# Performance work log

Hardware: AMD Instinct MI355X
Metric: run time of the kernel (lower is better)

Reference implementation:

```python
import jax, jax.numpy as jnp
import numpy as np

# Loihi neuron constants (from netParams['neuron'])
VTH_MANT = 80.0
THETA = VTH_MANT * 64.0          # Loihi threshold = vThMant * 2**6
I_DECAY = 1024.0                 # current decay (of 4096)
V_DECAY = 128.0                  # voltage decay (of 4096)
REF_DELAY = 1.0                  # refractory steps after a spike
W_SCALE = 64.0                   # Loihi weighted-input scaling (2**6)
TAU_RHO = 1.0
POOL_W = 1.1 * VTH_MANT          # slayer pool synapse weight (one spike fires output)


@jax.custom_vjp
def spike(v):
    return (v >= THETA).astype(v.dtype)

def _spike_fwd(v):
    return spike(v), v

def _spike_bwd(v, g):
    # SLAYER surrogate gradient: exponential pdf around threshold
    return (g * jnp.exp(-jnp.abs(v - THETA) / (TAU_RHO * THETA)) / THETA,)

spike.defvjp(_spike_fwd, _spike_bwd)


def loihi_dynamics(wsum):
    """CUBA Loihi LIF over time-leading weighted input wsum: [T, ...] -> spikes [T, ...]."""
    i_dec = (4096.0 - I_DECAY) / 4096.0
    v_dec = (4096.0 - V_DECAY) / 4096.0

    def step(carry, x):
        u, v, ref = carry
        u = i_dec * u + W_SCALE * x                    # synaptic current
        v = jnp.where(ref > 0, 0.0, v_dec * v + u)     # membrane, clamped in refractory
        s = spike(v)
        v = v * (1.0 - s)                              # reset on spike
        ref = jnp.where(s > 0, REF_DELAY, jnp.maximum(ref - 1.0, 0.0))
        return (u, v, ref), s

    z = jnp.zeros_like(wsum[0])
    _, s = jax.lax.scan(step, (z, z, z), wsum)
    return s


def delay_shift(s):
    # slayer.delayShift(spike, 1): shift spike train by 1 timestep (time-leading axis)
    return jnp.concatenate([jnp.zeros_like(s[:1]), s[:-1]], axis=0)


def conv2d_t(x, w, pad):
    # x: [T, B, C, H, W]; fold T into batch for the spatial conv
    T, B, C, H, W = x.shape
    y = jax.lax.conv_general_dilated(
        x.reshape(T * B, C, H, W), w, (1, 1), [(pad, pad), (pad, pad)],
        dimension_numbers=('NCHW', 'OIHW', 'NCHW'))
    return y.reshape(T, B, y.shape[1], y.shape[2], y.shape[3])


def sum_pool(x, k):
    # slayer pool: per-channel sum pooling with fixed synaptic weight POOL_W
    y = jax.lax.reduce_window(x, 0.0, jax.lax.add,
                              (1, 1, 1, k, k), (1, 1, 1, k, k), 'VALID')
    return POOL_W * y


def setup_inputs() -> dict:
    key = jax.random.key(0)
    ks = jax.random.split(key, 6)
    B, C, H, W, T = 48, 4, 26, 26, 128
    # Bernoulli(0.1) spike trains
    spike_input = (jax.random.uniform(ks[0], (B, C, H, W, T)) < 0.1).astype(jnp.float32)
    w_conv1 = jax.random.normal(ks[1], (8, 4, 5, 5), jnp.float32) * 4.0
    w_conv2 = jax.random.normal(ks[2], (16, 8, 3, 3), jnp.float32) * 4.0
    w_conv3 = jax.random.normal(ks[3], (32, 16, 3, 3), jnp.float32) * 4.0
    w_fc1 = jax.random.normal(ks[4], (512, 3 * 3 * 32), jnp.float32) * 4.0
    w_fc2 = jax.random.normal(ks[5], (2, 512), jnp.float32) * 4.0
    return {"spike_input": spike_input, "w_conv1": w_conv1, "w_conv2": w_conv2,
            "w_conv3": w_conv3, "w_fc1": w_fc1, "w_fc2": w_fc2}


def reference(spike_input, w_conv1, w_conv2, w_conv3, w_fc1, w_fc2):
    x = jnp.transpose(spike_input, (4, 0, 1, 2, 3))  # [T, B, C, H, W]

    def block(x, w, pad):
        s = delay_shift(loihi_dynamics(conv2d_t(x, w, pad)))
        s = delay_shift(loihi_dynamics(sum_pool(s, 2)))
        return s  # dropout is identity in eval

    x = block(x, w_conv1, 1)   # 26 -> 24 -> 12
    x = block(x, w_conv2, 1)   # 12 -> 12 -> 6
    x = block(x, w_conv3, 1)   # 6 -> 6 -> 3
    T, B = x.shape[0], x.shape[1]
    x = x.reshape(T, B, -1)    # [T, B, 32*3*3] (C,H,W flatten order matches torch view)
    s = delay_shift(loihi_dynamics(jnp.einsum('tbi,oi->tbo', x, w_fc1)))
    s = delay_shift(loihi_dynamics(jnp.einsum('tbi,oi->tbo', s, w_fc2)))
    return jnp.transpose(s, (1, 2, 0))  # [B, 2, T]
```

## Files before the change

kernel.cpp:

```cpp
#include <hip/hip_runtime.h>


#define THETA 5120.0f

typedef __attribute__((ext_vector_type(8))) short bfrag;
typedef __attribute__((ext_vector_type(4))) float ffrag;

__device__ __forceinline__ float dyn_step(float x, float& u, float& v, float& r) {
#pragma clang fp contract(off)
    u = 0.75f * u + 64.0f * x;
    float vn = 0.96875f * v + u;
    vn = (r > 0.0f) ? 0.0f : vn;
    float s;
    if (vn >= THETA) { s = 1.0f; v = 0.0f; r = 1.0f; }
    else             { s = 0.0f; v = vn; r = fmaxf(r - 1.0f, 0.0f); }
    return s;
}

__device__ __forceinline__ float dpp_add_xor1(float x) {
    int y = __builtin_amdgcn_update_dpp(0, __float_as_int(x), 0xB1, 0xF, 0xF, true);
    return x + __int_as_float(y);
}
__device__ __forceinline__ float dpp_add_xor2(float x) {
    int y = __builtin_amdgcn_update_dpp(0, __float_as_int(x), 0x4E, 0xF, 0xF, true);
    return x + __int_as_float(y);
}

__device__ __forceinline__ unsigned int compress4(unsigned long long x) {
    x &= 0x1111111111111111ull;
    x = (x | (x >> 3))  & 0x0303030303030303ull;
    x = (x | (x >> 6))  & 0x000F000F000F000Full;
    x = (x | (x >> 12)) & 0x000000FF000000FFull;
    x = (x | (x >> 24)) & 0xFFFFull;
    return (unsigned int)x;
}

__device__ __forceinline__ unsigned short f2bf(float f) {
    unsigned int u = __float_as_uint(f);
    unsigned int r = (u + 0x7FFFu + ((u >> 16) & 1u)) >> 16;
    return (unsigned short)r;
}
__device__ __forceinline__ float bf2f(unsigned short b) {
    return __uint_as_float(((unsigned int)b) << 16);
}

__device__ __forceinline__ float f4_elem(float4 v, int j) {
    return (j == 0) ? v.x : (j == 1) ? v.y : (j == 2) ? v.z : v.w;
}

__global__ __launch_bounds__(256) void k_masks(const float* __restrict__ in,
                                               const float* __restrict__ wfc1,
                                               uint2* __restrict__ xb,
                                               unsigned short* __restrict__ wb) {
    if (blockIdx.x >= 624) {
        int gid = (blockIdx.x - 624) * 256 + threadIdx.x;
        int o = gid / 288, k = gid % 288;
        float w = wfc1[gid];
        unsigned short b0 = f2bf(w);
        float r1 = w - bf2f(b0);
        unsigned short b1 = f2bf(r1);
        float r2 = r1 - bf2f(b1);
        unsigned short b2 = f2bf(r2);
        size_t ob = (size_t)o * 864 + k;
        wb[ob]       = b0;
        wb[ob + 288] = b1;
        wb[ob + 576] = b2;
        return;
    }
    int wv = blockIdx.x * 4 + (threadIdx.x >> 6);
    int lane = threadIdx.x & 63;
    int y = wv % 26; int r = wv / 26;
    int pr = r & 1; int b = r >> 1;
    int ch = lane >> 5;
    int x = lane & 31;
    int act = x < 26;
    int xc = act ? x : 25;
    const float4* src = (const float4*)(in + (size_t)(((b * 4 + pr * 2 + ch) * 26 + y) * 26 + xc) * 128);
    uint2* dst = xb + ((size_t)b * 2 + pr) * 28 + (y + 1);
    if (y == 0) {
        uint2* pp = xb + ((size_t)b * 2 + pr) * 28;
        uint2 z = make_uint2(0u, 0u);
#pragma unroll
        for (int h = 0; h < 2; ++h) {
            int t = h * 64 + lane;
            pp[(size_t)t * 2688] = z;
            pp[(size_t)t * 2688 + 27] = z;
        }
    }
    for (int t4 = 0; t4 < 32; ++t4) {
        float4 f = src[t4];
#pragma unroll
        for (int k = 0; k < 4; ++k) {
            float fv = f4_elem(f, k);
            unsigned long long bal = __ballot(act && (fv != 0.0f));
            if (lane == 0) {
                unsigned int lo = ((unsigned int)bal & 0x03FFFFFFu) << 1;
                unsigned int hi = ((unsigned int)(bal >> 32) & 0x03FFFFFFu) << 1;
                dst[(size_t)(t4 * 4 + k) * 2688] = make_uint2(lo, hi);
            }
        }
    }
}

__global__ __launch_bounds__(576) void k_wsum1(const uint2* __restrict__ xb,
                                               const float* __restrict__ w1,
                                               float* __restrict__ ws) {
    __shared__ float wsh[400];
    __shared__ ffrag tbl4[660];
    int tid = threadIdx.x;
    int H = blockIdx.x & 1;
    int bid = blockIdx.x >> 1;
    int tch = bid & 15;
    int b = bid >> 4;
    float* wsH = ws + (size_t)H * 14155776;
    if (tid < 400) wsh[tid] = w1[H * 400 + tid];
    __syncthreads();
    for (int e = tid; e < 660; e += 576) {
        int ch = e / 165;
        int rem = e % 165;
        int ky = rem / 33;
        int idx = rem % 33;
        ffrag val = {0.f, 0.f, 0.f, 0.f};
#pragma unroll
        for (int oc4 = 0; oc4 < 4; ++oc4) {
            float a = 0.f;
#pragma unroll
            for (int k = 0; k < 5; ++k)
                a += ((idx >> k) & 1) ? wsh[oc4 * 100 + ch * 25 + ky * 5 + k] : 0.f;
            val[oc4] = a;
        }
        tbl4[(ch * 5 + ky) * 33 + idx] = val;
    }
    __syncthreads();
    int q = tid >> 2, s = tid & 3;
    int ox = (q % 12) * 2 + (s & 1);
    int oy = (q / 12) * 2 + (s >> 1);
    int t0 = tch * 8;
    ffrag acc[8];
#pragma unroll
    for (int j = 0; j < 8; ++j) {
        int t = t0 + j;
        const uint2* rp = xb + ((size_t)t * 48 + b) * 56 + oy;
        ffrag a = {0.f, 0.f, 0.f, 0.f};
#pragma unroll
        for (int ky = 0; ky < 5; ++ky) {
            uint2 r0 = rp[ky];
            uint2 r1 = rp[28 + ky];
            a += tbl4[ky * 33 + (int)((r0.x >> ox) & 31u)];
            a += tbl4[(5 + ky) * 33 + (int)((r0.y >> ox) & 31u)];
            a += tbl4[(10 + ky) * 33 + (int)((r1.x >> ox) & 31u)];
            a += tbl4[(15 + ky) * 33 + (int)((r1.y >> ox) & 31u)];
        }
        acc[j] = a;
    }
    size_t tilebase = (size_t)(t0 >> 4) * 1769472 + (t0 & 15);
#pragma unroll
    for (int oc4 = 0; oc4 < 4; ++oc4) {
        float* wp = wsH + tilebase + (size_t)((b * 4 + oc4) * 576 + tid) * 16;
        *(float4*)(wp)     = make_float4(acc[0][oc4], acc[1][oc4], acc[2][oc4], acc[3][oc4]);
        *(float4*)(wp + 4) = make_float4(acc[4][oc4], acc[5][oc4], acc[6][oc4], acc[7][oc4]);
    }
}

__global__ __launch_bounds__(256) void k_scan1(const float* __restrict__ ws,
                                               unsigned short* __restrict__ st1) {
    int wv = blockIdx.x * 4 + (threadIdx.x >> 6);
    int lane = threadIdx.x & 63;
    int H = (wv >= 1728) ? 1 : 0;
    int wvl = wv - H * 1728;
    const float* bp = ws + (size_t)H * 14155776 + (size_t)(wvl * 64 + lane) * 16;
    unsigned short* so = st1 + (size_t)wv * 128;
    float u = 0.f, v = 0.f, rf = 0.f;
    float pu = 0.f, pv = 0.f, prf = 0.f;
    float sp = 0.f;
    unsigned int mb[4];
    float4 cur[4], nxt[4];
#pragma unroll
    for (int i = 0; i < 4; ++i) cur[i] = *(const float4*)(bp + i * 4);
    for (int tb = 0; tb < 8; ++tb) {
        if (tb < 7) {
            const float* np = bp + (size_t)(tb + 1) * 1769472;
#pragma unroll
            for (int i = 0; i < 4; ++i) nxt[i] = *(const float4*)(np + i * 4);
        }
#pragma unroll
        for (int j = 0; j < 16; ++j) {
            int t = tb * 16 + j;
            float w = f4_elem(cur[j >> 2], j & 3);
            float cnt = dpp_add_xor2(dpp_add_xor1(sp));
            float ps = dyn_step(88.0f * cnt, pu, pv, prf);
            unsigned long long bal = __ballot(((lane & 3) == 0) && (ps > 0.5f));
            unsigned int m = compress4(bal);
            int sl = (t >> 1) & 3;
            mb[sl] = (t & 1) ? (mb[sl] | (m << 16)) : m;
            if ((t & 7) == 7 && lane == 0)
                *(uint4*)(so + (t & ~7)) = make_uint4(mb[0], mb[1], mb[2], mb[3]);
            sp = dyn_step(w, u, v, rf);
        }
        if (tb < 7) {
#pragma unroll
            for (int i = 0; i < 4; ++i) cur[i] = nxt[i];
        }
    }
}

__global__ __launch_bounds__(256) void k_mb1(const unsigned short* __restrict__ st1,
                                             unsigned short* __restrict__ pb16) {
    int gid = blockIdx.x * 256 + threadIdx.x;
    int oc = gid & 7; int r = gid >> 3;
    int y = r % 12; r /= 12;
    int b = r % 48; int t = r / 48;
    int base = (oc >> 2) * 1728 + (b * 4 + (oc & 3)) * 9;
    int Q0 = y * 12;
    int w0 = Q0 >> 4, off = Q0 & 15;
    unsigned int v0 = st1[(size_t)(base + w0) * 128 + t];
    unsigned int v1 = (off > 4) ? (unsigned int)st1[(size_t)(base + w0 + 1) * 128 + t] : 0u;
    unsigned int m = ((v0 >> off) | (v1 << (16 - off))) & 0xFFFu;
    size_t rowb = (size_t)(t * 48 + b) * 14;
    pb16[(rowb + y + 1) * 8 + oc] = (unsigned short)(m << 1);
    if (y == 0)  pb16[rowb * 8 + oc] = 0;
    if (y == 11) pb16[(rowb + 13) * 8 + oc] = 0;
}

__global__ __launch_bounds__(576) void k_wsum2(const unsigned short* __restrict__ pb16,
                                               const float* __restrict__ w2,
                                               float* __restrict__ ws) {
    __shared__ float wsh[288];
    __shared__ ffrag tbl4[852];
    int tid = threadIdx.x;
    int tch = blockIdx.x & 3;
    int r = blockIdx.x >> 2;
    int ocg = r & 3; int b = r >> 2;
    if (tid < 288) wsh[tid] = w2[(ocg * 4 + tid / 72) * 72 + (tid % 72)];
    __syncthreads();
    for (int e = tid; e < 852; e += 576) {
        int pr = e / 213;
        int rem = e % 213;
        int ky = rem / 71;
        int idx = rem % 71;
        int lo = idx % 9, hi = idx / 9;
        ffrag val = {0.f, 0.f, 0.f, 0.f};
#pragma unroll
        for (int oc4 = 0; oc4 < 4; ++oc4) {
            float a = 0.f;
#pragma unroll
            for (int k = 0; k < 3; ++k)
                a += ((lo >> k) & 1) ? wsh[oc4 * 72 + (2 * pr) * 9 + ky * 3 + k] : 0.f;
#pragma unroll
            for (int k = 0; k < 3; ++k)
                a += ((hi >> k) & 1) ? wsh[oc4 * 72 + (2 * pr + 1) * 9 + ky * 3 + k] : 0.f;
            val[oc4] = a;
        }
        tbl4[(pr * 3 + ky) * 71 + idx] = val;
    }
    __syncthreads();
    int tq = tid / 144;
    int pix = tid % 144;
    int q = pix >> 2, s = pix & 3;
    int ox = (q % 6) * 2 + (s & 1);
    int oy = (q / 6) * 2 + (s >> 1);
    int t0 = tch * 32 + tq * 8;
    ffrag acc[8];
#pragma unroll
    for (int j = 0; j < 8; ++j) {
        int t = t0 + j;
        ffrag a = {0.f, 0.f, 0.f, 0.f};
        if (t > 0) {
            const uint4* rp = (const uint4*)(pb16 + (((size_t)(t - 1) * 48 + b) * 14 + oy) * 8);
#pragma unroll
            for (int ky = 0; ky < 3; ++ky) {
                uint4 row = rp[ky];
                unsigned int wd[4] = {row.x, row.y, row.z, row.w};
#pragma unroll
                for (int pr = 0; pr < 4; ++pr) {
                    unsigned int lo = (wd[pr] >> ox) & 7u;
                    unsigned int hi = (wd[pr] >> (16 + ox)) & 7u;
                    a += tbl4[(pr * 3 + ky) * 71 + (int)(lo + 9u * hi)];
                }
            }
        }
        acc[j] = a;
    }
    size_t tilebase = (size_t)(t0 >> 4) * 1769472 + (t0 & 15);
#pragma unroll
    for (int oc4 = 0; oc4 < 4; ++oc4) {
        int neuron = (b * 16 + ocg * 4 + oc4) * 144 + pix;
        float* wp = ws + tilebase + (size_t)neuron * 16;
        *(float4*)(wp)     = make_float4(acc[0][oc4], acc[1][oc4], acc[2][oc4], acc[3][oc4]);
        *(float4*)(wp + 4) = make_float4(acc[4][oc4], acc[5][oc4], acc[6][oc4], acc[7][oc4]);
    }
}

__global__ __launch_bounds__(576) void k_scan2(const float* __restrict__ ws,
                                               unsigned short* __restrict__ st2) {
    int tid = threadIdx.x;
    int wloc = tid >> 6, lane = tid & 63;
    int g4 = blockIdx.x;
    const float* bp = ws + (size_t)(g4 * 576 + tid) * 16;
    unsigned short* so = st2 + ((size_t)(g4 * 9 + wloc)) * 128;
    float u = 0.f, v = 0.f, rf = 0.f;
    float pu = 0.f, pv = 0.f, prf = 0.f;
    float sp = 0.f;
    unsigned int mb[4];
    float4 cur[4], nxt[4];
#pragma unroll
    for (int i = 0; i < 4; ++i) cur[i] = *(const float4*)(bp + i * 4);
    for (int tb = 0; tb < 8; ++tb) {
        if (tb < 7) {
            const float* np = bp + (size_t)(tb + 1) * 1769472;
#pragma unroll
            for (int i = 0; i < 4; ++i) nxt[i] = *(const float4*)(np + i * 4);
        }
#pragma unroll
        for (int j = 0; j < 16; ++j) {
            int t = tb * 16 + j;
            float w = f4_elem(cur[j >> 2], j & 3);
            float cnt = dpp_add_xor2(dpp_add_xor1(sp));
            float ps = dyn_step(88.0f * cnt, pu, pv, prf);
            unsigned long long bal = __ballot(((lane & 3) == 0) && (ps > 0.5f));
            unsigned int m = compress4(bal);
            int sl = (t >> 1) & 3;
            mb[sl] = (t & 1) ? (mb[sl] | (m << 16)) : m;
            if ((t & 7) == 7 && lane == 0)
                *(uint4*)(so + (t & ~7)) = make_uint4(mb[0], mb[1], mb[2], mb[3]);
            sp = dyn_step(w, u, v, rf);
        }
        if (tb < 7) {
#pragma unroll
            for (int i = 0; i < 4; ++i) cur[i] = nxt[i];
        }
    }
}

__global__ __launch_bounds__(256) void k_mb2(const unsigned short* __restrict__ st2,
                                             unsigned short* __restrict__ pb2) {
    int gid = blockIdx.x * 256 + threadIdx.x;
    int oc = gid & 15; int r = gid >> 4;
    int y = r % 6; r /= 6;
    int b = r % 48; int t = r / 48;
    int img = b * 16 + oc;
    int g4 = img >> 2, lI = img & 3;
    int Q0 = lI * 36 + y * 6;
    int w0 = Q0 >> 4, off = Q0 & 15;
    unsigned int v0 = st2[(size_t)(g4 * 9 + w0) * 128 + t];
    unsigned int v1 = (off > 10) ? (unsigned int)st2[(size_t)(g4 * 9 + w0 + 1) * 128 + t] : 0u;
    unsigned int m = ((v0 >> off) | (v1 << (16 - off))) & 0x3Fu;
    size_t rowb = (size_t)(t * 48 + b) * 8;
    pb2[(rowb + y + 1) * 16 + oc] = (unsigned short)(m << 1);
    if (y == 0) pb2[rowb * 16 + oc] = 0;
    if (y == 5) pb2[(rowb + 7) * 16 + oc] = 0;
}

__global__ __launch_bounds__(576) void k_wsum3(const unsigned short* __restrict__ pb2,
                                               const float* __restrict__ w3,
                                               float* __restrict__ ws) {
    __shared__ float wsh[576];
    __shared__ ffrag tbl4[1704];
    int tid = threadIdx.x;
    int tch = blockIdx.x & 7;
    int gb = blockIdx.x >> 3;
    int ocg = gb / 12, bg = gb % 12;
    wsh[tid] = w3[(ocg * 4 + tid / 144) * 144 + (tid % 144)];
    __syncthreads();
    for (int e = tid; e < 1536; e += 576) {
        int pr = e / 192;
        int ky = (e / 64) % 3;
        int i = e & 63;
        int lo = i & 7, hi = i >> 3;
        ffrag val = {0.f, 0.f, 0.f, 0.f};
#pragma unroll
        for (int oc4 = 0; oc4 < 4; ++oc4) {
            float a = 0.f;
#pragma unroll
            for (int k = 0; k < 3; ++k)
                a += ((lo >> k) & 1) ? wsh[oc4 * 144 + (2 * pr) * 9 + ky * 3 + k] : 0.f;
#pragma unroll
            for (int k = 0; k < 3; ++k)
                a += ((hi >> k) & 1) ? wsh[oc4 * 144 + (2 * pr + 1) * 9 + ky * 3 + k] : 0.f;
            val[oc4] = a;
        }
        tbl4[(pr * 3 + ky) * 71 + lo + 9 * hi] = val;
    }
    __syncthreads();
    int tq = tid & 3;
    int r = tid >> 2;
    int pix = r % 36;
    int bsel = r / 36;
    int q = pix >> 2, s = pix & 3;
    int ox = (q % 3) * 2 + (s & 1);
    int oy = (q / 3) * 2 + (s >> 1);
    int b = bg * 4 + bsel;
    int t0 = tch * 16 + tq * 4;
    ffrag acc[4];
#pragma unroll
    for (int j = 0; j < 4; ++j) {
        int t = t0 + j;
        ffrag a = {0.f, 0.f, 0.f, 0.f};
        if (t > 0) {
            const uint4* rp = (const uint4*)(pb2 + (((size_t)(t - 1) * 48 + b) * 8 + oy) * 16);
#pragma unroll
            for (int ky = 0; ky < 3; ++ky) {
                uint4 rA = rp[ky * 2];
                uint4 rB = rp[ky * 2 + 1];
                unsigned int wd[8] = {rA.x, rA.y, rA.z, rA.w, rB.x, rB.y, rB.z, rB.w};
#pragma unroll
                for (int pr = 0; pr < 8; ++pr) {
                    unsigned int lo = (wd[pr] >> ox) & 7u;
                    unsigned int hi = (wd[pr] >> (16 + ox)) & 7u;
                    a += tbl4[(pr * 3 + ky) * 71 + (int)(lo + 9u * hi)];
                }
            }
        }
        acc[j] = a;
    }
    size_t base = (size_t)tch * 884736;
#pragma unroll
    for (int oc4 = 0; oc4 < 4; ++oc4) {
        int neuron = (b * 32 + ocg * 4 + oc4) * 36 + pix;
        float* wp = ws + base + (size_t)neuron * 16 + tq * 4;
        *(float4*)(wp) = make_float4(acc[0][oc4], acc[1][oc4], acc[2][oc4], acc[3][oc4]);
    }
}

__global__ __launch_bounds__(256) void k_scan3(const float* __restrict__ ws,
                                               unsigned short* __restrict__ st3) {
    int wv = blockIdx.x * 4 + (threadIdx.x >> 6);
    int lane = threadIdx.x & 63;
    const float* bp = ws + (size_t)(wv * 64 + lane) * 16;
    unsigned short* so = st3 + (size_t)wv * 128;
    float u = 0.f, v = 0.f, rf = 0.f;
    float pu = 0.f, pv = 0.f, prf = 0.f;
    float sp = 0.f;
    unsigned int mb[4];
    float4 cur[4], nxt[4];
#pragma unroll
    for (int i = 0; i < 4; ++i) cur[i] = *(const float4*)(bp + i * 4);
    for (int tb = 0; tb < 8; ++tb) {
        if (tb < 7) {
            const float* np = bp + (size_t)(tb + 1) * 884736;
#pragma unroll
            for (int i = 0; i < 4; ++i) nxt[i] = *(const float4*)(np + i * 4);
        }
#pragma unroll
        for (int j = 0; j < 16; ++j) {
            int t = tb * 16 + j;
            float w = f4_elem(cur[j >> 2], j & 3);
            float cnt = dpp_add_xor2(dpp_add_xor1(sp));
            float ps = dyn_step(88.0f * cnt, pu, pv, prf);
            unsigned long long bal = __ballot(((lane & 3) == 0) && (ps > 0.5f));
            unsigned int m = compress4(bal);
            int sl = (t >> 1) & 3;
            mb[sl] = (t & 1) ? (mb[sl] | (m << 16)) : m;
            if ((t & 7) == 7 && lane == 0)
                *(uint4*)(so + (t & ~7)) = make_uint4(mb[0], mb[1], mb[2], mb[3]);
            sp = dyn_step(w, u, v, rf);
        }
        if (tb < 7) {
#pragma unroll
            for (int i = 0; i < 4; ++i) cur[i] = nxt[i];
        }
    }
}

__global__ __launch_bounds__(256) void k_mb3(const unsigned short* __restrict__ st3,
                                             unsigned short* __restrict__ a3) {
    int gid = blockIdx.x * 256 + threadIdx.x;
    if (gid >= 1755648) return;
    int G = gid % 13824, t = gid / 13824;
    unsigned int bit = ((unsigned int)st3[(size_t)(G >> 4) * 128 + t] >> (G & 15)) & 1u;
    a3[(size_t)(t + 1) * 13824 + G] = bit ? 0x3F80 : 0;
    if (gid < 13824) a3[gid] = 0;
}

__global__ __launch_bounds__(256) void k_fc1mm(const unsigned short* __restrict__ a3,
                                               const unsigned short* __restrict__ wb,
                                               float* __restrict__ wsf1) {
    __shared__ unsigned short Bs[16 * 872];
    int tid = threadIdx.x;
    int nt = blockIdx.x & 31;
    int mc = blockIdx.x >> 5;
    int n0 = nt * 16;
    for (int idx = tid; idx < 13824; idx += 256) {
        int n = idx / 864;
        int kp = idx % 864;
        Bs[n * 872 + kp] = wb[(size_t)(n0 + n) * 864 + kp];
    }
    __syncthreads();
    int wave = tid >> 6;
    int lane = tid & 63;
    int ln = lane & 15, quad = lane >> 4;
#pragma unroll
    for (int i = 0; i < 4; ++i) {
        int m0 = (mc * 16 + wave * 4 + i) * 16;
        const unsigned short* arow = a3 + (size_t)(m0 + ln) * 288 + quad * 8;
        ffrag acc = {0.f, 0.f, 0.f, 0.f};
#pragma unroll
        for (int kb = 0; kb < 9; ++kb) {
            bfrag av = *(const bfrag*)(arow + kb * 32);
#pragma unroll
            for (int c = 0; c < 3; ++c) {
                bfrag bv = *(const bfrag*)(&Bs[ln * 872 + c * 288 + kb * 32 + quad * 8]);
                acc = __builtin_amdgcn_mfma_f32_16x16x32_bf16(av, bv, acc, 0, 0, 0);
            }
        }
        float* wout = wsf1 + (size_t)(m0 + quad * 4) * 512 + n0 + ln;
        wout[0] = acc[0];
        wout[512] = acc[1];
        wout[1024] = acc[2];
        wout[1536] = acc[3];
    }
}

__global__ __launch_bounds__(256) void k_fc1s(const float* __restrict__ wsf1,
                                              float* __restrict__ f1f) {
    int tid = blockIdx.x * 256 + threadIdx.x;
    float u = 0.f, v = 0.f, rf = 0.f;
    float wbuf[16];
#pragma unroll
    for (int i = 0; i < 16; ++i) wbuf[i] = wsf1[(size_t)i * 24576 + tid];
    for (int tb = 0; tb < 128; tb += 16) {
#pragma unroll
        for (int j = 0; j < 16; ++j) {
            int t = tb + j;
            float w = wbuf[j];
            if (t + 16 < 128) wbuf[j] = wsf1[(size_t)(t + 16) * 24576 + tid];
            float s = dyn_step(w, u, v, rf);
            f1f[(size_t)t * 24576 + tid] = s;
        }
    }
}

__global__ __launch_bounds__(256) void k_fc2w(const float* __restrict__ f1f,
                                              const float* __restrict__ wfc2,
                                              float* __restrict__ wsf2) {
    int wv = blockIdx.x * 4 + (threadIdx.x >> 6);
    int lane = threadIdx.x & 63;
    int b = wv % 48, t = wv / 48;
    int o = lane & 1, kq = lane >> 1;
    float acc = 0.f;
    if (t > 0) {
        const float* wp = wfc2 + o * 512 + kq * 16;
        const float* sp = f1f + (size_t)(t - 1) * 24576 + b * 512 + kq * 16;
#pragma unroll
        for (int i = 0; i < 16; ++i) acc += wp[i] * sp[i];
    }
#pragma unroll
    for (int m = 2; m < 64; m <<= 1) acc += __shfl_xor(acc, m, 64);
    if (lane < 2) wsf2[(size_t)t * 96 + b * 2 + o] = acc;
}

__global__ __launch_bounds__(128) void k_fc2s(const float* __restrict__ wsf2,
                                              float* __restrict__ out) {
    int tid = threadIdx.x;
    if (tid >= 96) return;
    float* ob = out + tid * 128;
    ob[0] = 0.0f;
    float u = 0.f, v = 0.f, rf = 0.f;
    float wbuf[8];
#pragma unroll
    for (int i = 0; i < 8; ++i) wbuf[i] = wsf2[(size_t)i * 96 + tid];
    for (int tb = 0; tb < 128; tb += 8) {
#pragma unroll
        for (int j = 0; j < 8; ++j) {
            int t = tb + j;
            float w = wbuf[j];
            if (t + 8 < 128) wbuf[j] = wsf2[(size_t)(t + 8) * 96 + tid];
            float s = dyn_step(w, u, v, rf);
            if (t < 127) ob[t + 1] = s;
        }
    }
}

extern "C" void kernel_launch(void* const* d_in, const int* in_sizes, int n_in,
                              void* d_out, int out_size, void* d_ws, size_t ws_size,
                              hipStream_t stream) {
    const float* in   = (const float*)d_in[0];
    const float* w1   = (const float*)d_in[1];
    const float* w2   = (const float*)d_in[2];
    const float* w3   = (const float*)d_in[3];
    const float* wfc1 = (const float*)d_in[4];
    const float* wfc2 = (const float*)d_in[5];
    float* out = (float*)d_out;
    char* ws = (char*)d_ws;

    float*          slab = (float*)(ws);
    uint2*          xb   = (uint2*)(ws + 113246208);
    unsigned short* pb16 = (unsigned short*)(ws + 115998720);
    unsigned short* pb2  = (unsigned short*)(ws + 117374976);
    float*          f1f  = (float*)(ws + 118947840);
    unsigned short* a3   = (unsigned short*)(ws + 131530752);
    unsigned short* wb   = (unsigned short*)(ws + 135069696);
    unsigned short* st1  = (unsigned short*)(ws + 135954432);
    unsigned short* st2  = (unsigned short*)(ws + 136839168);
    unsigned short* st3  = (unsigned short*)(ws + 137281536);
    float*          wsf1 = (float*)(ws);
    float*          wsf2 = (float*)(ws + 16777216);

    k_masks   <<<1200, 256, 0, stream>>>(in, wfc1, xb, wb);
    k_wsum1   <<<1536, 576, 0, stream>>>(xb, w1, slab);
    k_scan1   <<<864, 256, 0, stream>>>(slab, st1);
    k_mb1     <<<2304, 256, 0, stream>>>(st1, pb16);
    k_wsum2   <<<768, 576, 0, stream>>>(pb16, w2, slab);
    k_scan2   <<<192, 576, 0, stream>>>(slab, st2);
    k_mb2     <<<2304, 256, 0, stream>>>(st2, pb2);
    k_wsum3   <<<768, 576, 0, stream>>>(pb2, w3, slab);
    k_scan3   <<<216, 256, 0, stream>>>(slab, st3);
    k_mb3     <<<6858, 256, 0, stream>>>(st3, a3);
    k_fc1mm   <<<768, 256, 0, stream>>>(a3, wb, wsf1);
    k_fc1s    <<<96, 256, 0, stream>>>(wsf1, f1f);
    k_fc2w    <<<1536, 256, 0, stream>>>(f1f, wfc2, wsf2);
    k_fc2s    <<<1, 128, 0, stream>>>(wsf2, out);
}
```

Baseline: 375.5 us.

## Fuse spike-mask repacking kernels into scan kernels via shared memory

Each scan kernel now writes its packed spike bitmasks into shared memory and, after a block barrier, repacks them directly into the padded layout consumed by the next conv stage (or the bf16 FC1 input). This removes three separate repack kernels, their launches, and the global round trip through the st1/st2/st3 buffers. The scan1 grid is regrouped into 576-thread blocks so that each block holds all 9 waves of one image/channel. The tail repacking loop adds some serialized work after the scan within each block.

```diff
diff --git a/kernel.cpp b/kernel.cpp
--- a/kernel.cpp
+++ b/kernel.cpp
@@ -162,14 +162,17 @@
     }
 }
 
-__global__ __launch_bounds__(256) void k_scan1(const float* __restrict__ ws,
-                                               unsigned short* __restrict__ st1) {
-    int wv = blockIdx.x * 4 + (threadIdx.x >> 6);
-    int lane = threadIdx.x & 63;
-    int H = (wv >= 1728) ? 1 : 0;
-    int wvl = wv - H * 1728;
-    const float* bp = ws + (size_t)H * 14155776 + (size_t)(wvl * 64 + lane) * 16;
-    unsigned short* so = st1 + (size_t)wv * 128;
+__global__ __launch_bounds__(576) void k_scan1(const float* __restrict__ ws,
+                                               unsigned short* __restrict__ pb16) {
+    __shared__ unsigned short sh[9 * 128];
+    int tid = threadIdx.x;
+    int sub = tid >> 6, lane = tid & 63;
+    int blk = blockIdx.x;
+    int H = (blk >= 192) ? 1 : 0;
+    int ibl = blk - H * 192;
+    int b = ibl >> 2, ocl = ibl & 3;
+    int oc = H * 4 + ocl;
+    const float* bp = ws + (size_t)H * 14155776 + (size_t)((ibl * 9 + sub) * 64 + lane) * 16;
     float u = 0.f, v = 0.f, rf = 0.f;
     float pu = 0.f, pv = 0.f, prf = 0.f;
     float sp = 0.f;
@@ -194,7 +197,7 @@
             int sl = (t >> 1) & 3;
             mb[sl] = (t & 1) ? (mb[sl] | (m << 16)) : m;
             if ((t & 7) == 7 && lane == 0)
-                *(uint4*)(so + (t & ~7)) = make_uint4(mb[0], mb[1], mb[2], mb[3]);
+                *(uint4*)(&sh[sub * 128 + (t & ~7)]) = make_uint4(mb[0], mb[1], mb[2], mb[3]);
             sp = dyn_step(w, u, v, rf);
         }
         if (tb < 7) {
@@ -202,24 +205,19 @@
             for (int i = 0; i < 4; ++i) cur[i] = nxt[i];
         }
     }
-}
-
-__global__ __launch_bounds__(256) void k_mb1(const unsigned short* __restrict__ st1,
-                                             unsigned short* __restrict__ pb16) {
-    int gid = blockIdx.x * 256 + threadIdx.x;
-    int oc = gid & 7; int r = gid >> 3;
-    int y = r % 12; r /= 12;
-    int b = r % 48; int t = r / 48;
-    int base = (oc >> 2) * 1728 + (b * 4 + (oc & 3)) * 9;
-    int Q0 = y * 12;
-    int w0 = Q0 >> 4, off = Q0 & 15;
-    unsigned int v0 = st1[(size_t)(base + w0) * 128 + t];
-    unsigned int v1 = (off > 4) ? (unsigned int)st1[(size_t)(base + w0 + 1) * 128 + t] : 0u;
-    unsigned int m = ((v0 >> off) | (v1 << (16 - off))) & 0xFFFu;
-    size_t rowb = (size_t)(t * 48 + b) * 14;
-    pb16[(rowb + y + 1) * 8 + oc] = (unsigned short)(m << 1);
-    if (y == 0)  pb16[rowb * 8 + oc] = 0;
-    if (y == 11) pb16[(rowb + 13) * 8 + oc] = 0;
+    __syncthreads();
+    for (int idx = tid; idx < 1536; idx += 576) {
+        int t = idx / 12, y = idx % 12;
+        int Q0 = y * 12;
+        int w0 = Q0 >> 4, off = Q0 & 15;
+        unsigned int v0 = sh[w0 * 128 + t];
+        unsigned int v1 = (off > 4) ? (unsigned int)sh[(w0 + 1) * 128 + t] : 0u;
+        unsigned int m = ((v0 >> off) | (v1 << (16 - off))) & 0xFFFu;
+        size_t rowb = (size_t)(t * 48 + b) * 14;
+        pb16[(rowb + y + 1) * 8 + oc] = (unsigned short)(m << 1);
+        if (y == 0)  pb16[rowb * 8 + oc] = 0;
+        if (y == 11) pb16[(rowb + 13) * 8 + oc] = 0;
+    }
 }
 
 __global__ __launch_bounds__(576) void k_wsum2(const unsigned short* __restrict__ pb16,
@@ -292,12 +290,12 @@
 }
 
 __global__ __launch_bounds__(576) void k_scan2(const float* __restrict__ ws,
-                                               unsigned short* __restrict__ st2) {
+                                               unsigned short* __restrict__ pb2) {
+    __shared__ unsigned short sh[9 * 128];
     int tid = threadIdx.x;
     int wloc = tid >> 6, lane = tid & 63;
     int g4 = blockIdx.x;
     const float* bp = ws + (size_t)(g4 * 576 + tid) * 16;
-    unsigned short* so = st2 + ((size_t)(g4 * 9 + wloc)) * 128;
     float u = 0.f, v = 0.f, rf = 0.f;
     float pu = 0.f, pv = 0.f, prf = 0.f;
     float sp = 0.f;
@@ -322,7 +320,7 @@
             int sl = (t >> 1) & 3;
             mb[sl] = (t & 1) ? (mb[sl] | (m << 16)) : m;
             if ((t & 7) == 7 && lane == 0)
-                *(uint4*)(so + (t & ~7)) = make_uint4(mb[0], mb[1], mb[2], mb[3]);
+                *(uint4*)(&sh[wloc * 128 + (t & ~7)]) = make_uint4(mb[0], mb[1], mb[2], mb[3]);
             sp = dyn_step(w, u, v, rf);
         }
         if (tb < 7) {
@@ -330,25 +328,23 @@
             for (int i = 0; i < 4; ++i) cur[i] = nxt[i];
         }
     }
-}
-
-__global__ __launch_bounds__(256) void k_mb2(const unsigned short* __restrict__ st2,
-                                             unsigned short* __restrict__ pb2) {
-    int gid = blockIdx.x * 256 + threadIdx.x;
-    int oc = gid & 15; int r = gid >> 4;
-    int y = r % 6; r /= 6;
-    int b = r % 48; int t = r / 48;
-    int img = b * 16 + oc;
-    int g4 = img >> 2, lI = img & 3;
-    int Q0 = lI * 36 + y * 6;
-    int w0 = Q0 >> 4, off = Q0 & 15;
-    unsigned int v0 = st2[(size_t)(g4 * 9 + w0) * 128 + t];
-    unsigned int v1 = (off > 10) ? (unsigned int)st2[(size_t)(g4 * 9 + w0 + 1) * 128 + t] : 0u;
-    unsigned int m = ((v0 >> off) | (v1 << (16 - off))) & 0x3Fu;
-    size_t rowb = (size_t)(t * 48 + b) * 8;
-    pb2[(rowb + y + 1) * 16 + oc] = (unsigned short)(m << 1);
-    if (y == 0) pb2[rowb * 16 + oc] = 0;
-    if (y == 5) pb2[(rowb + 7) * 16 + oc] = 0;
+    __syncthreads();
+    for (int idx = tid; idx < 3072; idx += 576) {
+        int t = idx / 24;
+        int r2 = idx % 24;
+        int lI = r2 / 6, y = r2 % 6;
+        int img = g4 * 4 + lI;
+        int b = img >> 4, oc = img & 15;
+        int Q0 = lI * 36 + y * 6;
+        int w0 = Q0 >> 4, off = Q0 & 15;
+        unsigned int v0 = sh[w0 * 128 + t];
+        unsigned int v1 = (off > 10) ? (unsigned int)sh[(w0 + 1) * 128 + t] : 0u;
+        unsigned int m = ((v0 >> off) | (v1 << (16 - off))) & 0x3Fu;
+        size_t rowb = (size_t)(t * 48 + b) * 8;
+        pb2[(rowb + y + 1) * 16 + oc] = (unsigned short)(m << 1);
+        if (y == 0) pb2[rowb * 16 + oc] = 0;
+        if (y == 5) pb2[(rowb + 7) * 16 + oc] = 0;
+    }
 }
 
 __global__ __launch_bounds__(576) void k_wsum3(const unsigned short* __restrict__ pb2,
@@ -423,11 +419,12 @@
 }
 
 __global__ __launch_bounds__(256) void k_scan3(const float* __restrict__ ws,
-                                               unsigned short* __restrict__ st3) {
-    int wv = blockIdx.x * 4 + (threadIdx.x >> 6);
-    int lane = threadIdx.x & 63;
+                                               unsigned short* __restrict__ a3) {
+    __shared__ unsigned short sh[4 * 128];
+    int tid = threadIdx.x;
+    int wloc = tid >> 6, lane = tid & 63;
+    int wv = blockIdx.x * 4 + wloc;
     const float* bp = ws + (size_t)(wv * 64 + lane) * 16;
-    unsigned short* so = st3 + (size_t)wv * 128;
     float u = 0.f, v = 0.f, rf = 0.f;
     float pu = 0.f, pv = 0.f, prf = 0.f;
     float sp = 0.f;
@@ -452,7 +449,7 @@
             int sl = (t >> 1) & 3;
             mb[sl] = (t & 1) ? (mb[sl] | (m << 16)) : m;
             if ((t & 7) == 7 && lane == 0)
-                *(uint4*)(so + (t & ~7)) = make_uint4(mb[0], mb[1], mb[2], mb[3]);
+                *(uint4*)(&sh[wloc * 128 + (t & ~7)]) = make_uint4(mb[0], mb[1], mb[2], mb[3]);
             sp = dyn_step(w, u, v, rf);
         }
         if (tb < 7) {
@@ -460,16 +457,14 @@
             for (int i = 0; i < 4; ++i) cur[i] = nxt[i];
         }
     }
-}
-
-__global__ __launch_bounds__(256) void k_mb3(const unsigned short* __restrict__ st3,
-                                             unsigned short* __restrict__ a3) {
-    int gid = blockIdx.x * 256 + threadIdx.x;
-    if (gid >= 1755648) return;
-    int G = gid % 13824, t = gid / 13824;
-    unsigned int bit = ((unsigned int)st3[(size_t)(G >> 4) * 128 + t] >> (G & 15)) & 1u;
-    a3[(size_t)(t + 1) * 13824 + G] = bit ? 0x3F80 : 0;
-    if (gid < 13824) a3[gid] = 0;
+    __syncthreads();
+    int G0 = blockIdx.x * 64;
+    int g = tid & 63, tq = tid >> 6;
+    if (tq == 0) a3[G0 + g] = 0;
+    for (int t = tq; t < 127; t += 4) {
+        unsigned int bit = ((unsigned int)sh[(g >> 4) * 128 + t] >> (g & 15)) & 1u;
+        a3[(size_t)(t + 1) * 13824 + G0 + g] = bit ? 0x3F80 : 0;
+    }
 }
 
 __global__ __launch_bounds__(256) void k_fc1mm(const unsigned short* __restrict__ a3,
@@ -590,22 +585,16 @@
     float*          f1f  = (float*)(ws + 118947840);
     unsigned short* a3   = (unsigned short*)(ws + 131530752);
     unsigned short* wb   = (unsigned short*)(ws + 135069696);
-    unsigned short* st1  = (unsigned short*)(ws + 135954432);
-    unsigned short* st2  = (unsigned short*)(ws + 136839168);
-    unsigned short* st3  = (unsigned short*)(ws + 137281536);
     float*          wsf1 = (float*)(ws);
     float*          wsf2 = (float*)(ws + 16777216);
 
     k_masks   <<<1200, 256, 0, stream>>>(in, wfc1, xb, wb);
     k_wsum1   <<<1536, 576, 0, stream>>>(xb, w1, slab);
-    k_scan1   <<<864, 256, 0, stream>>>(slab, st1);
-    k_mb1     <<<2304, 256, 0, stream>>>(st1, pb16);
+    k_scan1   <<<384, 576, 0, stream>>>(slab, pb16);
     k_wsum2   <<<768, 576, 0, stream>>>(pb16, w2, slab);
-    k_scan2   <<<192, 576, 0, stream>>>(slab, st2);
-    k_mb2     <<<2304, 256, 0, stream>>>(st2, pb2);
+    k_scan2   <<<192, 576, 0, stream>>>(slab, pb2);
     k_wsum3   <<<768, 576, 0, stream>>>(pb2, w3, slab);
-    k_scan3   <<<216, 256, 0, stream>>>(slab, st3);
-    k_mb3     <<<6858, 256, 0, stream>>>(st3, a3);
+    k_scan3   <<<216, 256, 0, stream>>>(slab, a3);
     k_fc1mm   <<<768, 256, 0, stream>>>(a3, wb, wsf1);
     k_fc1s    <<<96, 256, 0, stream>>>(wsf1, f1f);
     k_fc2w    <<<1536, 256, 0, stream>>>(f1f, wfc2, wsf2);
```

Result: no change. 371.2 us (median of 3 runs) (-1.2%).
